# Optimization experiments

Hardware: AMD Instinct MI355X
Metric: run time of the kernel (lower is better)

Reference implementation:

```python
import jax, jax.numpy as jnp
import numpy as np

FP8_MAX = 448.0
SCALE_EPS = 1e-6


def setup_inputs() -> dict:
    key = jax.random.key(0)
    k1, k2, k3 = jax.random.split(key, 3)
    B, S, D_IN, D_OUT = 4, 2048, 4096, 4096
    x = jax.random.normal(k1, (B, S, D_IN), dtype=jnp.float32)
    weight = jax.random.normal(k2, (D_OUT, D_IN), dtype=jnp.float32) * 0.02
    bias = jax.random.normal(k3, (D_OUT,), dtype=jnp.float32) * 0.01
    return {"x": x, "weight": weight, "bias": bias}


def _quantize_weight(weight):
    # per-output-row amax -> scale (computed in fp32, stored via fp16 round-trip as in _quantize_weight)
    w = weight.astype(jnp.float32)
    max_abs = jnp.max(jnp.abs(w), axis=1, keepdims=True)          # [out, 1]
    scale = jnp.maximum(max_abs / FP8_MAX, SCALE_EPS)
    scale = scale.astype(jnp.float16).astype(jnp.float32)          # fp16 storage of scale, copied back to fp32 buffer
    w_fp8 = jnp.clip(w / scale, -FP8_MAX, FP8_MAX).astype(jnp.float8_e4m3fn)
    return w_fp8, scale


def reference(x, weight, bias):
    out_features, in_features = weight.shape
    w_fp8, w_scale = _quantize_weight(weight)                      # [out,in] fp8, [out,1] f32

    x2d = x.reshape(-1, in_features)                               # [T, in]
    act_abs = jnp.max(jnp.abs(x2d), axis=1, keepdims=True)         # per-row amax [T,1]
    act_scale = jnp.maximum(act_abs / FP8_MAX, SCALE_EPS).astype(jnp.float32)
    x_fp8 = jnp.clip(x2d / act_scale.astype(x.dtype), -FP8_MAX, FP8_MAX).astype(jnp.float8_e4m3fn)

    # torch._scaled_mm: (x_fp8 @ w_fp8^T) * act_scale * weight_scale^T + bias(bf16), out in bf16
    acc = jnp.matmul(x_fp8.astype(jnp.float32), w_fp8.astype(jnp.float32).T)  # [T, out]
    out = acc * act_scale * w_scale.T
    out = out + bias.astype(jnp.bfloat16).astype(jnp.float32)
    out = out.astype(jnp.bfloat16).astype(x.dtype)
    return out.reshape(*x.shape[:-1], out_features)
```

## Files before the change

### kernel.cpp

```cpp
#include <hip/hip_runtime.h>
#include <hip/hip_fp16.h>
#include <stdint.h>

#define FP8_MAX_V 448.0f
#define BM 128
#define BN 128
#define BKB 128

typedef float floatx4 __attribute__((ext_vector_type(4)));
typedef int intx4 __attribute__((ext_vector_type(4)));
typedef int intx8 __attribute__((ext_vector_type(8)));

#define WAITVM(n)                                              \
  do {                                                         \
    asm volatile("s_waitcnt vmcnt(" #n ")" ::: "memory");      \
    __builtin_amdgcn_sched_barrier(0);                         \
  } while (0)
#define BARRIER()                                              \
  do {                                                         \
    __builtin_amdgcn_sched_barrier(0);                         \
    __builtin_amdgcn_s_barrier();                              \
    __builtin_amdgcn_sched_barrier(0);                         \
  } while (0)

__device__ __forceinline__ float bf16_rne(float v) {
  uint32_t u = __float_as_uint(v);
  u = (u + 0x7fffu + ((u >> 16) & 1u)) & 0xffff0000u;
  return __uint_as_float(u);
}

__device__ __forceinline__ uint32_t pack4_fp8(float a, float b, float c, float d) {
  int p = 0;
  p = __builtin_amdgcn_cvt_pk_fp8_f32(a, b, p, false);
  p = __builtin_amdgcn_cvt_pk_fp8_f32(c, d, p, true);
  return (uint32_t)p;
}

__device__ __forceinline__ void gload_lds16(const uint8_t* g, uint8_t* l) {
  __builtin_amdgcn_global_load_lds(
      (const __attribute__((address_space(1))) uint32_t*)g,
      (__attribute__((address_space(3))) uint32_t*)l,
      16, 0, 0);
}

__global__ __launch_bounds__(256) void quant_all_kernel(
    const float* __restrict__ x, const float* __restrict__ w,
    uint8_t* __restrict__ x8, uint8_t* __restrict__ w8,
    float* __restrict__ asc, float* __restrict__ wsc, int M, int K) {
  const int blk = blockIdx.x;
  const bool isW = blk >= M;
  const int row = isW ? (blk - M) : blk;
  const float* rp = (isW ? w : x) + (size_t)row * K;
  uint8_t* out8 = (isW ? w8 : x8) + (size_t)row * K;
  float* scp = (isW ? wsc : asc) + row;
  const int tid = threadIdx.x;

  float4 v[4];
  float amax = 0.f;
#pragma unroll
  for (int i = 0; i < 4; ++i) {
    v[i] = ((const float4*)rp)[i * 256 + tid];
    amax = fmaxf(amax, fmaxf(fmaxf(fabsf(v[i].x), fabsf(v[i].y)),
                             fmaxf(fabsf(v[i].z), fabsf(v[i].w))));
  }
#pragma unroll
  for (int off = 32; off; off >>= 1) amax = fmaxf(amax, __shfl_xor(amax, off));
  __shared__ float red[4];
  if ((tid & 63) == 0) red[tid >> 6] = amax;
  __syncthreads();
  amax = fmaxf(fmaxf(red[0], red[1]), fmaxf(red[2], red[3]));

  float scale = fmaxf(amax / FP8_MAX_V, 1e-6f);
  if (isW) scale = __half2float(__float2half(scale));
  if (tid == 0) *scp = scale;

  uint32_t* op = (uint32_t*)out8;
#pragma unroll
  for (int i = 0; i < 4; ++i) {
    float qa = fminf(fmaxf(v[i].x / scale, -FP8_MAX_V), FP8_MAX_V);
    float qb = fminf(fmaxf(v[i].y / scale, -FP8_MAX_V), FP8_MAX_V);
    float qc = fminf(fmaxf(v[i].z / scale, -FP8_MAX_V), FP8_MAX_V);
    float qd = fminf(fmaxf(v[i].w / scale, -FP8_MAX_V), FP8_MAX_V);
    op[i * 256 + tid] = pack4_fp8(qa, qb, qc, qd);
  }
}

__global__ __launch_bounds__(256, 2) void gemm_fp8_kernel(
    const uint8_t* __restrict__ A8, const uint8_t* __restrict__ B8,
    const float* __restrict__ asc, const float* __restrict__ wsc,
    const float* __restrict__ bias, float* __restrict__ out,
    int M, int N, int K) {
  __shared__ __align__(16) uint8_t As[2][BM * BKB];
  __shared__ __align__(16) uint8_t Bs[BN * BKB];

  const int tid = threadIdx.x;
  const int lane = tid & 63;
  const int wid = tid >> 6;
  const int wr = wid >> 1;
  const int wc = wid & 1;

  const int ntn = N / BN;
  const int bm = blockIdx.x / ntn;
  const int bn = blockIdx.x % ntn;

  floatx4 acc[4][4] = {};

  const int srow = tid >> 3;
  const int sc_log = (tid & 7) ^ (srow & 7);
  const uint8_t* ga0 = A8 + (size_t)(bm * BM + srow) * K + sc_log * 16;
  const uint8_t* gb0 = B8 + (size_t)(bn * BN + srow) * K + sc_log * 16;
  const size_t rstep = (size_t)32 * K;

  const int fr = lane & 15;
  const int hi = lane >> 4;
  const int fsw = fr & 7;
  const int cls = ((2 * hi) ^ fsw) * 16;
  const int chs = ((2 * hi + 1) ^ fsw) * 16;

  auto stageA = [&](int buf, int k0) {
    uint8_t* lA = As[buf] + tid * 16;
#pragma unroll
    for (int i = 0; i < 4; ++i) gload_lds16(ga0 + i * rstep + k0, lA + i * 4096);
  };
  auto stageB = [&](int k0) {
    uint8_t* lB = Bs + tid * 16;
#pragma unroll
    for (int i = 0; i < 4; ++i) gload_lds16(gb0 + i * rstep + k0, lB + i * 4096);
  };

  auto compute = [&](int buf) {
    const uint8_t* Ab = As[buf];
    intx8 a[4], b[4];
#pragma unroll
    for (int m = 0; m < 4; ++m) {
      const uint8_t* p = Ab + (size_t)(wr * 64 + m * 16 + fr) * BKB;
      intx4 lo = *(const intx4*)(p + cls);
      intx4 hh = *(const intx4*)(p + chs);
      a[m] = (intx8){lo.x, lo.y, lo.z, lo.w, hh.x, hh.y, hh.z, hh.w};
    }
#pragma unroll
    for (int n = 0; n < 4; ++n) {
      const uint8_t* p = Bs + (size_t)(wc * 64 + n * 16 + fr) * BKB;
      intx4 lo = *(const intx4*)(p + cls);
      intx4 hh = *(const intx4*)(p + chs);
      b[n] = (intx8){lo.x, lo.y, lo.z, lo.w, hh.x, hh.y, hh.z, hh.w};
    }
#pragma unroll
    for (int m = 0; m < 4; ++m)
#pragma unroll
      for (int n = 0; n < 4; ++n)
        acc[m][n] = __builtin_amdgcn_mfma_scale_f32_16x16x128_f8f6f4(
            a[m], b[n], acc[m][n], 0, 0, 0, 0x7F7F7F7F, 0, 0x7F7F7F7F);
  };

  const int NT = K / BKB;
  stageA(0, 0);
  stageB(0);
  stageA(1, BKB);

  for (int t = 0; t < NT; ++t) {
    if (t + 1 < NT) WAITVM(4); else WAITVM(0);
    BARRIER();
    compute(t & 1);
    BARRIER();
    if (t + 1 < NT) stageB((t + 1) * BKB);
    if (t + 2 < NT) stageA(t & 1, (t + 2) * BKB);
  }

  const int rbase = bm * BM + wr * 64;
  const int cbase = bn * BN + wc * 64;
#pragma unroll
  for (int n = 0; n < 4; ++n) {
    const int col = cbase + n * 16 + fr;
    const float wv = wsc[col];
    const float bb = bf16_rne(bias[col]);
#pragma unroll
    for (int m = 0; m < 4; ++m) {
      const int r0 = rbase + m * 16 + hi * 4;
#pragma unroll
      for (int r = 0; r < 4; ++r) {
        const int row = r0 + r;
        float v = (acc[m][n][r] * asc[row]) * wv + bb;
        out[(size_t)row * N + col] = bf16_rne(v);
      }
    }
  }
}

extern "C" void kernel_launch(void* const* d_in, const int* in_sizes, int n_in,
                              void* d_out, int out_size, void* d_ws, size_t ws_size,
                              hipStream_t stream) {
  const float* x = (const float*)d_in[0];
  const float* w = (const float*)d_in[1];
  const float* bias = (const float*)d_in[2];
  float* out = (float*)d_out;

  const int N = in_sizes[2];
  const int K = in_sizes[1] / N;
  const int M = in_sizes[0] / K;

  uint8_t* x8 = (uint8_t*)d_ws;
  uint8_t* w8 = x8 + (size_t)M * K;
  float* asc = (float*)(w8 + (size_t)N * K);
  float* wsc = asc + M;
  (void)ws_size; (void)n_in; (void)out_size;

  quant_all_kernel<<<M + N, 256, 0, stream>>>(x, w, x8, w8, asc, wsc, M, K);
  gemm_fp8_kernel<<<(M / BM) * (N / BN), 256, 0, stream>>>(x8, w8, asc, wsc, bias, out, M, N, K);
}
```

Before: 193.5 us.

## Enlarge GEMM tile to 256x256 with 8 waves and double-buffered B

```diff
diff --git a/kernel.cpp b/kernel.cpp
--- a/kernel.cpp
+++ b/kernel.cpp
@@ -3,8 +3,8 @@
 #include <stdint.h>
 
 #define FP8_MAX_V 448.0f
-#define BM 128
-#define BN 128
+#define BM 256
+#define BN 256
 #define BKB 128
 
 typedef float floatx4 __attribute__((ext_vector_type(4)));
@@ -85,31 +85,31 @@
   }
 }
 
-__global__ __launch_bounds__(256, 2) void gemm_fp8_kernel(
+__global__ __launch_bounds__(512, 2) void gemm_fp8_kernel(
     const uint8_t* __restrict__ A8, const uint8_t* __restrict__ B8,
     const float* __restrict__ asc, const float* __restrict__ wsc,
     const float* __restrict__ bias, float* __restrict__ out,
     int M, int N, int K) {
   __shared__ __align__(16) uint8_t As[2][BM * BKB];
-  __shared__ __align__(16) uint8_t Bs[BN * BKB];
+  __shared__ __align__(16) uint8_t Bs[2][BN * BKB];
 
   const int tid = threadIdx.x;
   const int lane = tid & 63;
   const int wid = tid >> 6;
-  const int wr = wid >> 1;
-  const int wc = wid & 1;
+  const int wr = wid >> 2;
+  const int wc = wid & 3;
 
   const int ntn = N / BN;
   const int bm = blockIdx.x / ntn;
   const int bn = blockIdx.x % ntn;
 
-  floatx4 acc[4][4] = {};
+  floatx4 acc[8][4] = {};
 
   const int srow = tid >> 3;
   const int sc_log = (tid & 7) ^ (srow & 7);
-  const uint8_t* ga0 = A8 + (size_t)(bm * BM + srow) * K + sc_log * 16;
-  const uint8_t* gb0 = B8 + (size_t)(bn * BN + srow) * K + sc_log * 16;
-  const size_t rstep = (size_t)32 * K;
+  const uint8_t* gA = A8 + (size_t)(bm * BM + srow) * K + sc_log * 16;
+  const uint8_t* gB = B8 + (size_t)(bn * BN + srow) * K + sc_log * 16;
+  const size_t rstep = (size_t)64 * K;
 
   const int fr = lane & 15;
   const int hi = lane >> 4;
@@ -120,54 +120,71 @@
   auto stageA = [&](int buf, int k0) {
     uint8_t* lA = As[buf] + tid * 16;
 #pragma unroll
-    for (int i = 0; i < 4; ++i) gload_lds16(ga0 + i * rstep + k0, lA + i * 4096);
-  };
-  auto stageB = [&](int k0) {
-    uint8_t* lB = Bs + tid * 16;
-#pragma unroll
-    for (int i = 0; i < 4; ++i) gload_lds16(gb0 + i * rstep + k0, lB + i * 4096);
-  };
-
-  auto compute = [&](int buf) {
-    const uint8_t* Ab = As[buf];
-    intx8 a[4], b[4];
+    for (int i = 0; i < 4; ++i) gload_lds16(gA + i * rstep + k0, lA + i * 8192);
+  };
+  auto stageB = [&](int buf, int k0) {
+    uint8_t* lB = Bs[buf] + tid * 16;
+#pragma unroll
+    for (int i = 0; i < 4; ++i) gload_lds16(gB + i * rstep + k0, lB + i * 8192);
+  };
+
+  auto loadA = [&](intx8* a, int buf, int mh) {
 #pragma unroll
     for (int m = 0; m < 4; ++m) {
-      const uint8_t* p = Ab + (size_t)(wr * 64 + m * 16 + fr) * BKB;
+      const uint8_t* p = As[buf] + (size_t)(wr * 128 + (mh * 4 + m) * 16 + fr) * BKB;
       intx4 lo = *(const intx4*)(p + cls);
       intx4 hh = *(const intx4*)(p + chs);
       a[m] = (intx8){lo.x, lo.y, lo.z, lo.w, hh.x, hh.y, hh.z, hh.w};
     }
+  };
+  auto loadB = [&](intx8* b, int buf) {
 #pragma unroll
     for (int n = 0; n < 4; ++n) {
-      const uint8_t* p = Bs + (size_t)(wc * 64 + n * 16 + fr) * BKB;
+      const uint8_t* p = Bs[buf] + (size_t)(wc * 64 + n * 16 + fr) * BKB;
       intx4 lo = *(const intx4*)(p + cls);
       intx4 hh = *(const intx4*)(p + chs);
       b[n] = (intx8){lo.x, lo.y, lo.z, lo.w, hh.x, hh.y, hh.z, hh.w};
     }
+  };
+
+  const int NT = K / BKB;
+  stageA(0, 0);
+  stageB(0, 0);
+
+  for (int t = 0; t < NT; ++t) {
+    const int cur = t & 1, nxt = cur ^ 1;
+    WAITVM(0);
+    BARRIER();
+
+    intx8 a[4], b[4];
+    loadB(b, cur);
+    loadA(a, cur, 0);
+    if (t + 1 < NT) stageA(nxt, (t + 1) * BKB);
+    BARRIER();
+    __builtin_amdgcn_s_setprio(1);
 #pragma unroll
     for (int m = 0; m < 4; ++m)
 #pragma unroll
       for (int n = 0; n < 4; ++n)
         acc[m][n] = __builtin_amdgcn_mfma_scale_f32_16x16x128_f8f6f4(
             a[m], b[n], acc[m][n], 0, 0, 0, 0x7F7F7F7F, 0, 0x7F7F7F7F);
-  };
-
-  const int NT = K / BKB;
-  stageA(0, 0);
-  stageB(0);
-  stageA(1, BKB);
-
-  for (int t = 0; t < NT; ++t) {
-    if (t + 1 < NT) WAITVM(4); else WAITVM(0);
-    BARRIER();
-    compute(t & 1);
-    BARRIER();
-    if (t + 1 < NT) stageB((t + 1) * BKB);
-    if (t + 2 < NT) stageA(t & 1, (t + 2) * BKB);
-  }
-
-  const int rbase = bm * BM + wr * 64;
+    __builtin_amdgcn_s_setprio(0);
+    BARRIER();
+
+    loadA(a, cur, 1);
+    if (t + 1 < NT) stageB(nxt, (t + 1) * BKB);
+    BARRIER();
+    __builtin_amdgcn_s_setprio(1);
+#pragma unroll
+    for (int m = 0; m < 4; ++m)
+#pragma unroll
+      for (int n = 0; n < 4; ++n)
+        acc[4 + m][n] = __builtin_amdgcn_mfma_scale_f32_16x16x128_f8f6f4(
+            a[m], b[n], acc[4 + m][n], 0, 0, 0, 0x7F7F7F7F, 0, 0x7F7F7F7F);
+    __builtin_amdgcn_s_setprio(0);
+  }
+
+  const int rbase = bm * BM + wr * 128;
   const int cbase = bn * BN + wc * 64;
 #pragma unroll
   for (int n = 0; n < 4; ++n) {
@@ -175,7 +192,7 @@
     const float wv = wsc[col];
     const float bb = bf16_rne(bias[col]);
 #pragma unroll
-    for (int m = 0; m < 4; ++m) {
+    for (int m = 0; m < 8; ++m) {
       const int r0 = rbase + m * 16 + hi * 4;
 #pragma unroll
       for (int r = 0; r < 4; ++r) {
@@ -206,5 +223,5 @@
   (void)ws_size; (void)n_in; (void)out_size;
 
   quant_all_kernel<<<M + N, 256, 0, stream>>>(x, w, x8, w8, asc, wsc, M, K);
-  gemm_fp8_kernel<<<(M / BM) * (N / BN), 256, 0, stream>>>(x8, w8, asc, wsc, bias, out, M, N, K);
-}
+  gemm_fp8_kernel<<<(M / BM) * (N / BN), 512, 0, stream>>>(x8, w8, asc, wsc, bias, out, M, N, K);
+}
```

Result: slower. 242.9 us (+25.5%).
